# Kernel tuning notes

Hardware: AMD Instinct MI355X
Metric: run time of the kernel (lower is better)

## Reference

```python
import jax, jax.numpy as jnp
import numpy as np

GAMMA = 0.96875
SCALE_BASE = 512.0


def _fixed_pos_embedding(scale):
    # scale: (L, d) where d = head_dim // 2
    L, d = scale.shape
    inv_freq = 1.0 / (10000.0 ** (jnp.arange(d, dtype=jnp.float32) / d))
    sinusoid = jnp.arange(L, dtype=jnp.float32)[:, None] * inv_freq  # (L, d)
    return jnp.sin(sinusoid), jnp.cos(sinusoid)


def _rotate_every_two(x):
    # (..., D) -> (..., D) with pairs (x0, x1) -> (-x1, x0)
    x1 = x[..., ::2]
    x2 = x[..., 1::2]
    return jnp.stack((-x2, x1), axis=-1).reshape(x.shape)


def _dup_interleave(m):
    # (L, d) -> (L, 2d), each column duplicated (matches rotary pairing)
    return jnp.repeat(m, 2, axis=-1)


def xpos(x, offset=0, downscale=False):
    # x: (B, S, D). Standard torchscale-style XPos rotary embedding.
    S, D = x.shape[-2], x.shape[-1]
    scale_vec = (jnp.arange(0, D, 2, dtype=jnp.float32) + 0.4 * D) / (1.4 * D)  # (D/2,)
    min_pos = -(S + offset) // 2
    max_pos = S + offset + min_pos
    power = jnp.arange(min_pos, max_pos, dtype=jnp.float32) / SCALE_BASE  # (S+offset,)
    scale = scale_vec ** power[:, None]  # (S+offset, D/2)
    sin, cos = _fixed_pos_embedding(scale)
    if scale.shape[0] > S:  # keep the last S positions
        scale, sin, cos = scale[-S:], sin[-S:], cos[-S:]
    if downscale:
        scale = 1.0 / scale
    sin = _dup_interleave(sin * scale)  # (S, D)
    cos = _dup_interleave(cos * scale)  # (S, D)
    return x * cos + _rotate_every_two(x) * sin


def _decay_mask(S, dtype):
    # D[n, m] = gamma^(n-m) if n >= m else 0  (lower triangular)
    m = jnp.arange(S)
    diff = m[:, None] - m  # (S, S)
    causal = diff >= 0
    exp = jnp.where(causal, diff, 0).astype(dtype)
    return jnp.where(causal, jnp.asarray(GAMMA, dtype) ** exp, jnp.zeros((), dtype))


def setup_inputs() -> dict:
    key = jax.random.key(0)
    kx, kq, kk, kv = jax.random.split(key, 4)
    B, S, H, Dh = 4, 4096, 2048, 256
    return {
        "x": jax.random.normal(kx, (B, S, H), dtype=jnp.float32),
        "w_q": jax.random.normal(kq, (H, Dh), dtype=jnp.float32),
        "w_k": jax.random.normal(kk, (H, Dh), dtype=jnp.float32),
        "w_v": jax.random.normal(kv, (H, Dh), dtype=jnp.float32),
    }


def reference(x, w_q, w_k, w_v):
    # x: (B, S, H) -> out: (B, S, Dh)
    B, S, _ = x.shape
    decay = _decay_mask(S, x.dtype)[None]  # (1, S, S)
    q = xpos(x @ w_q)                       # (B, S, Dh)
    k = xpos(x @ w_k, downscale=True)       # (B, S, Dh)
    v = x @ w_v                             # (B, S, Dh)
    ret = jnp.einsum("bsd,btd->bst", q, k) * decay  # (B, S, S)
    return jnp.einsum("bst,btd->bsd", ret, v)       # (B, S, Dh)
```

## Files before the change

kernel.cpp:

```cpp
#include <hip/hip_runtime.h>
#include <cstddef>
#include <cstdint>

#define Bn 4
#define Sn 4096
#define Hn 2048
#define Dn 256

typedef float f32x16 __attribute__((ext_vector_type(16)));
typedef short bf16x8 __attribute__((ext_vector_type(8)));

#define AS3 __attribute__((address_space(3)))
#define AS1 __attribute__((address_space(1)))

#define L2G -0.045803689613125f
#define GC 2.9526131e-4f

__device__ __forceinline__ unsigned short f2bf(float f) {
  union { float f; unsigned int u; } a; a.f = f;
  unsigned int r = a.u + 0x7fffu + ((a.u >> 16) & 1u);
  return (unsigned short)(r >> 16);
}
__device__ __forceinline__ float bf2f(unsigned int b) {
  union { unsigned int u; float f; } a; a.u = b << 16;
  return a.f;
}

__global__ __launch_bounds__(256) void prep_kernel(const float* __restrict__ wq,
                                                   const float* __restrict__ wk,
                                                   const float* __restrict__ wv,
                                                   unsigned short* __restrict__ wt,
                                                   float* __restrict__ rt) {
  __shared__ __align__(16) unsigned short T[64][72];
  const int bx = blockIdx.x;
  const int tid = threadIdx.x;
  if (bx < 2048) {
    const int g = bx * 256 + tid;
    const int s = g >> 7;
    const int jp = g & 127;
    const float invf = exp2f((float)jp * (-13.287712379549449f / 128.0f));
    float sn, cs;
    sincosf((float)s * invf, &sn, &cs);
    const float l2sv = log2f((2.0f * jp + 102.4f) * (1.0f / 358.4f));
    const float pw = ((float)s - 2048.0f) * (1.0f / 512.0f);
    const float tl = (float)(s & 255) * L2G;
    const float ex = pw * l2sv + tl;
    const float eq = exp2f(ex), ek = exp2f(-ex);
    float2* q = (float2*)rt;
    float2* k = (float2*)(rt + 4096 * 256);
    q[(size_t)s * 128 + jp] = make_float2(cs * eq, sn * eq);
    k[(size_t)s * 128 + jp] = make_float2(cs * ek, sn * ek);
  } else {
    const int bw = bx - 2048;
    const int k0 = (bw & 31) * 64;
    const int n0 = (bw >> 5) * 64;
    const float* w = (n0 < 256) ? wq : (n0 < 512 ? wk : wv);
    const int nc0 = n0 & 255;
#pragma unroll
    for (int it = 0; it < 2; ++it) {
      int flat = it * 256 + tid;
      int r = flat >> 3, c8 = flat & 7;
      const float* src = w + (size_t)(k0 + r) * 256 + nc0 + c8 * 8;
      float4 v0 = *(const float4*)src;
      float4 v1 = *(const float4*)(src + 4);
      T[c8 * 8 + 0][r] = f2bf(v0.x); T[c8 * 8 + 1][r] = f2bf(v0.y);
      T[c8 * 8 + 2][r] = f2bf(v0.z); T[c8 * 8 + 3][r] = f2bf(v0.w);
      T[c8 * 8 + 4][r] = f2bf(v1.x); T[c8 * 8 + 5][r] = f2bf(v1.y);
      T[c8 * 8 + 6][r] = f2bf(v1.z); T[c8 * 8 + 7][r] = f2bf(v1.w);
    }
    __syncthreads();
#pragma unroll
    for (int it = 0; it < 2; ++it) {
      int flat = it * 256 + tid;
      int nr = flat >> 3, kc8 = flat & 7;
      int n = n0 + nr;
      int kc_sw = kc8 ^ (n & 7);
      uint4 val = *(const uint4*)&T[nr][kc8 * 8];
      *(uint4*)((char*)wt + (size_t)n * 4096 + (size_t)k0 * 2 + kc_sw * 16) = val;
    }
  }
}

__global__ __launch_bounds__(512, 2) void proj6_kernel(const float* __restrict__ x,
                                                       const unsigned short* __restrict__ wt,
                                                       const float* __restrict__ rt,
                                                       unsigned short* __restrict__ qkv,
                                                       unsigned short* __restrict__ kt,
                                                       unsigned short* __restrict__ vt) {
  __shared__ __align__(16) char smem[49152];
  unsigned short* As = (unsigned short*)smem;
  const int tid = threadIdx.x;
  const int lane = tid & 63;
  const int wid = tid >> 6;
  const int wr = wid >> 2, wc = wid & 3;
  const int m0 = blockIdx.x * 128;
  const int kind = blockIdx.y;
  const int l31 = lane & 31, lh = lane >> 5;

  const int arow = tid >> 2;
  const int acg = (tid & 3) << 4;
  const int asw = (arow & 7) << 4;

  f32x16 acc[2][2];
#pragma unroll
  for (int i = 0; i < 2; ++i)
#pragma unroll
    for (int j = 0; j < 2; ++j) acc[i][j] = 0.0f;

  for (int k0 = 0; k0 < Hn; k0 += 64) {
    const float* srcA = x + (size_t)(m0 + arow) * 2048 + k0 + acg;
    float4 f0 = ((const float4*)srcA)[0];
    float4 f1 = ((const float4*)srcA)[1];
    float4 f2 = ((const float4*)srcA)[2];
    float4 f3 = ((const float4*)srcA)[3];
    {
      AS3 char* ldsb = (AS3 char*)(smem + 16384);
#pragma unroll
      for (int i = 0; i < 4; ++i) {
        int ou = i * 8192 + wid * 1024;
        int o = ou + lane * 16;
        int row = o >> 7, colB = o & 127;
        const char* srcB = (const char*)wt + (size_t)(kind * 256 + row) * 4096 + k0 * 2 + colB;
        __builtin_amdgcn_global_load_lds((const AS1 unsigned int*)srcB,
                                         (AS3 unsigned int*)(ldsb + ou), 16, 0, 0);
      }
    }
    {
      uint4 u0, u1;
      asm("v_cvt_pk_bf16_f32 %0, %1, %2" : "=v"(u0.x) : "v"(f0.x), "v"(f0.y));
      asm("v_cvt_pk_bf16_f32 %0, %1, %2" : "=v"(u0.y) : "v"(f0.z), "v"(f0.w));
      asm("v_cvt_pk_bf16_f32 %0, %1, %2" : "=v"(u0.z) : "v"(f1.x), "v"(f1.y));
      asm("v_cvt_pk_bf16_f32 %0, %1, %2" : "=v"(u0.w) : "v"(f1.z), "v"(f1.w));
      asm("v_cvt_pk_bf16_f32 %0, %1, %2" : "=v"(u1.x) : "v"(f2.x), "v"(f2.y));
      asm("v_cvt_pk_bf16_f32 %0, %1, %2" : "=v"(u1.y) : "v"(f2.z), "v"(f2.w));
      asm("v_cvt_pk_bf16_f32 %0, %1, %2" : "=v"(u1.z) : "v"(f3.x), "v"(f3.y));
      asm("v_cvt_pk_bf16_f32 %0, %1, %2" : "=v"(u1.w) : "v"(f3.z), "v"(f3.w));
      *(uint4*)((char*)As + arow * 128 + ((acg * 2) ^ asw)) = u0;
      *(uint4*)((char*)As + arow * 128 + ((acg * 2 + 16) ^ asw)) = u1;
    }
    __syncthreads();
#pragma unroll
    for (int kc = 0; kc < 4; ++kc) {
      const int kb = kc * 32 + lh * 16;
      bf16x8 a[2], b[2];
#pragma unroll
      for (int i = 0; i < 2; ++i) {
        int mr = wr * 64 + i * 32 + l31;
        a[i] = *(const bf16x8*)((const char*)As + mr * 128 + (kb ^ ((mr & 7) << 4)));
        int nr = wc * 64 + i * 32 + l31;
        b[i] = *(const bf16x8*)(smem + 16384 + nr * 128 + (kb ^ ((nr & 7) << 4)));
      }
#pragma unroll
      for (int i = 0; i < 2; ++i)
#pragma unroll
        for (int j = 0; j < 2; ++j)
          acc[i][j] = __builtin_amdgcn_mfma_f32_32x32x16_bf16(a[i], b[j], acc[i][j], 0, 0, 0);
    }
    __syncthreads();
  }

  const int bidx = m0 >> 12;
  const int t0b = m0 & 4095;

  if (kind < 2) {
    const float* rtb = rt + (size_t)kind * (4096 * 256);
    int jp[2];
#pragma unroll
    for (int j = 0; j < 2; ++j) jp[j] = (wc * 64 + j * 32 + l31) >> 1;
    const int odd = l31 & 1;
#pragma unroll
    for (int i = 0; i < 2; ++i)
#pragma unroll
      for (int reg = 0; reg < 16; ++reg) {
        const int mm = m0 + wr * 64 + i * 32 + (reg & 3) + 8 * (reg >> 2) + 4 * lh;
        const int s = mm & (Sn - 1);
#pragma unroll
        for (int j = 0; j < 2; ++j) {
          const float2 cf = *(const float2*)(rtb + (size_t)s * 256 + jp[j] * 2);
          float v = acc[i][j][reg];
          float p = __shfl_xor(v, 1, 64);
          acc[i][j][reg] = odd ? (v * cf.x + p * cf.y) : (v * cf.x - p * cf.y);
        }
      }
  }

  if (kind == 0) {
#pragma unroll
    for (int i = 0; i < 2; ++i)
#pragma unroll
      for (int j = 0; j < 2; ++j)
#pragma unroll
        for (int reg = 0; reg < 16; ++reg) {
          int m = m0 + wr * 64 + i * 32 + (reg & 3) + 8 * (reg >> 2) + 4 * lh;
          int n = wc * 64 + j * 32 + l31;
          qkv[(size_t)m * 768 + n] = f2bf(acc[i][j][reg]);
        }
  } else {
    if (kind == 1) {
#pragma unroll
      for (int i = 0; i < 2; ++i)
#pragma unroll
        for (int j = 0; j < 2; ++j)
#pragma unroll
          for (int reg = 0; reg < 16; ++reg) {
            int m = m0 + wr * 64 + i * 32 + (reg & 3) + 8 * (reg >> 2) + 4 * lh;
            int d = wc * 64 + j * 32 + l31;
            qkv[(size_t)m * 768 + 256 + (d ^ ((m & 7) << 3))] = f2bf(acc[i][j][reg]);
          }
    }
    unsigned short* dst = (kind == 1) ? kt : vt;
#pragma unroll
    for (int h = 0; h < 2; ++h) {
      __syncthreads();
      if ((wc >> 1) == h) {
#pragma unroll
        for (int i = 0; i < 2; ++i)
#pragma unroll
          for (int j = 0; j < 2; ++j) {
            const int dl = (wc & 1) * 64 + j * 32 + l31;
#pragma unroll
            for (int k8 = 0; k8 < 8; ++k8) {
              const int r0 = 2 * k8;
              const int t = wr * 64 + i * 32 + (r0 & 3) + 8 * (r0 >> 2) + 4 * lh;
              unsigned int pk;
              asm("v_cvt_pk_bf16_f32 %0, %1, %2" : "=v"(pk)
                  : "v"(acc[i][j][r0]), "v"(acc[i][j][r0 + 1]));
              *(unsigned int*)(smem + dl * 256 + ((2 * t) ^ ((dl & 7) << 4))) = pk;
            }
          }
      }
      __syncthreads();
#pragma unroll
      for (int p = 0; p < 4; ++p) {
        const int fl = p * 512 + tid;
        const int dl = fl >> 4, t8 = fl & 15;
        uint4 val = *(const uint4*)(smem + dl * 256 + ((t8 * 16) ^ ((dl & 7) << 4)));
        *(uint4*)(dst + (size_t)(bidx * 256 + h * 128 + dl) * 4096 + t0b + t8 * 8) = val;
      }
    }
  }
}

__global__ __launch_bounds__(256) void wt_build(const float* __restrict__ wq,
                                                const float* __restrict__ wk,
                                                const float* __restrict__ wv,
                                                unsigned short* __restrict__ wt) {
  __shared__ __align__(16) unsigned short T[64][72];
  const int tid = threadIdx.x;
  const int k0 = blockIdx.x * 64;
  const int n0 = blockIdx.y * 64;
  const float* w = (n0 < 256) ? wq : (n0 < 512 ? wk : wv);
  const int nc0 = n0 & 255;
#pragma unroll
  for (int it = 0; it < 2; ++it) {
    int flat = it * 256 + tid;
    int r = flat >> 3, c8 = flat & 7;
    const float* src = w + (size_t)(k0 + r) * 256 + nc0 + c8 * 8;
    float4 v0 = *(const float4*)src;
    float4 v1 = *(const float4*)(src + 4);
    T[c8 * 8 + 0][r] = f2bf(v0.x); T[c8 * 8 + 1][r] = f2bf(v0.y);
    T[c8 * 8 + 2][r] = f2bf(v0.z); T[c8 * 8 + 3][r] = f2bf(v0.w);
    T[c8 * 8 + 4][r] = f2bf(v1.x); T[c8 * 8 + 5][r] = f2bf(v1.y);
    T[c8 * 8 + 6][r] = f2bf(v1.z); T[c8 * 8 + 7][r] = f2bf(v1.w);
  }
  __syncthreads();
#pragma unroll
  for (int it = 0; it < 2; ++it) {
    int flat = it * 256 + tid;
    int nr = flat >> 3, kc8 = flat & 7;
    int n = n0 + nr;
    int kc_sw = kc8 ^ (n & 7);
    uint4 val = *(const uint4*)&T[nr][kc8 * 8];
    *(uint4*)((char*)wt + (size_t)n * 4096 + (size_t)k0 * 2 + kc_sw * 16) = val;
  }
}

__global__ __launch_bounds__(256, 2) void proj_kernel(const float* __restrict__ x,
                                                      const unsigned short* __restrict__ wt,
                                                      unsigned short* __restrict__ qkv) {
  __shared__ __align__(16) unsigned short As[128 * 64];
  __shared__ __align__(16) unsigned short Bs[128 * 64];
  const int tid = threadIdx.x;
  const int lane = tid & 63;
  const int wid = tid >> 6;
  const int wr = wid >> 1, wc = wid & 1;
  const int m0 = blockIdx.x * 128;
  const int n0 = blockIdx.y * 128;
  const int l31 = lane & 31, lh = lane >> 5;

  f32x16 acc[2][2];
#pragma unroll
  for (int i = 0; i < 2; ++i)
#pragma unroll
    for (int j = 0; j < 2; ++j) acc[i][j] = 0.0f;

  for (int k0 = 0; k0 < Hn; k0 += 64) {
    {
      AS3 char* ldsb = (AS3 char*)Bs;
#pragma unroll
      for (int i = 0; i < 4; ++i) {
        int ou = i * 4096 + wid * 1024;
        int o = ou + lane * 16;
        int row = o >> 7, col = o & 127;
        const char* src = (const char*)wt + (size_t)(n0 + row) * 4096 + k0 * 2 + col;
        __builtin_amdgcn_global_load_lds((const AS1 unsigned int*)src,
                                         (AS3 unsigned int*)(ldsb + ou), 16, 0, 0);
      }
    }
#pragma unroll
    for (int i = 0; i < 4; ++i) {
      int o = i * 256 + tid;
      int row = o >> 3, c8 = o & 7;
      const float* src = x + (size_t)(m0 + row) * 2048 + k0 + c8 * 8;
      float4 v0 = *(const float4*)src;
      float4 v1 = *(const float4*)(src + 4);
      uint4 val;
      val.x = f2bf(v0.x) | ((unsigned int)f2bf(v0.y) << 16);
      val.y = f2bf(v0.z) | ((unsigned int)f2bf(v0.w) << 16);
      val.z = f2bf(v1.x) | ((unsigned int)f2bf(v1.y) << 16);
      val.w = f2bf(v1.z) | ((unsigned int)f2bf(v1.w) << 16);
      *(uint4*)((char*)As + row * 128 + ((c8 * 16) ^ ((row & 7) << 4))) = val;
    }
    __syncthreads();
#pragma unroll
    for (int kc = 0; kc < 4; ++kc) {
      const int kb = kc * 32 + lh * 16;
      bf16x8 a[2], b[2];
#pragma unroll
      for (int i = 0; i < 2; ++i) {
        int mr = wr * 64 + i * 32 + l31;
        a[i] = *(const bf16x8*)((const char*)As + mr * 128 + (kb ^ ((mr & 7) << 4)));
        int nr = wc * 64 + i * 32 + l31;
        b[i] = *(const bf16x8*)((const char*)Bs + nr * 128 + (kb ^ ((nr & 7) << 4)));
      }
#pragma unroll
      for (int i = 0; i < 2; ++i)
#pragma unroll
        for (int j = 0; j < 2; ++j)
          acc[i][j] = __builtin_amdgcn_mfma_f32_32x32x16_bf16(a[i], b[j], acc[i][j], 0, 0, 0);
    }
    __syncthreads();
  }
  const bool khalf = (n0 >= 256 && n0 < 512);
#pragma unroll
  for (int i = 0; i < 2; ++i)
#pragma unroll
    for (int j = 0; j < 2; ++j)
#pragma unroll
      for (int reg = 0; reg < 16; ++reg) {
        int m = m0 + wr * 64 + i * 32 + (reg & 3) + 8 * (reg >> 2) + 4 * lh;
        int n = n0 + wc * 64 + j * 32 + l31;
        if (khalf) n = 256 + ((n - 256) ^ ((m & 7) << 3));
        qkv[(size_t)m * 768 + n] = f2bf(acc[i][j][reg]);
      }
}

__global__ __launch_bounds__(256) void xpos_kernel(unsigned short* __restrict__ qkv) {
  const int g = blockIdx.x * 256 + threadIdx.x;
  const int m = g >> 5;
  const int c = g & 31;
  const float s = (float)(m & (Sn - 1));
  unsigned short* qrow = qkv + (size_t)m * 768;
  const int csw = c ^ (m & 7);
  uint4 qv = *(uint4*)(qrow + c * 8);
  uint4 kv = *(uint4*)(qrow + 256 + csw * 8);
  unsigned int* qu = (unsigned int*)&qv;
  unsigned int* ku = (unsigned int*)&kv;
  const float pw = (s - 2048.0f) * (1.0f / 512.0f);
  const float gp = exp2f((float)(m & 255) * L2G);
#pragma unroll
  for (int p = 0; p < 4; ++p) {
    const int jp = c * 4 + p;
    const float invf = exp2f((float)jp * (-13.287712379549449f / 128.0f));
    float sn, cs;
    sincosf(s * invf, &sn, &cs);
    const float sv = (2.0f * jp + 102.4f) * (1.0f / 358.4f);
    const float scq = exp2f(pw * log2f(sv)) * gp;
    const float sci = 1.0f / scq;
    float q0 = bf2f(qu[p] & 0xffffu), q1 = bf2f(qu[p] >> 16);
    float k0 = bf2f(ku[p] & 0xffffu), k1 = bf2f(ku[p] >> 16);
    float q0r = (q0 * cs - q1 * sn) * scq;
    float q1r = (q1 * cs + q0 * sn) * scq;
    float k0r = (k0 * cs - k1 * sn) * sci;
    float k1r = (k1 * cs + k0 * sn) * sci;
    qu[p] = f2bf(q0r) | ((unsigned int)f2bf(q1r) << 16);
    ku[p] = f2bf(k0r) | ((unsigned int)f2bf(k1r) << 16);
  }
  *(uint4*)(qrow + c * 8) = qv;
  *(uint4*)(qrow + 256 + csw * 8) = kv;
}

__global__ __launch_bounds__(256) void kvt_build(const unsigned short* __restrict__ qkv,
                                                 unsigned short* __restrict__ kt,
                                                 unsigned short* __restrict__ vt) {
  __shared__ __align__(16) unsigned short Tk[64][72];
  __shared__ __align__(16) unsigned short Tv[64][72];
  const int tid = threadIdx.x;
  const int t0 = blockIdx.x * 64;
  const int d0 = blockIdx.y * 64;
  const int b = blockIdx.z;
  const size_t rowb = ((size_t)b * Sn + t0) * 1536;
#pragma unroll
  for (int it = 0; it < 2; ++it) {
    int flat = it * 256 + tid;
    int r = flat >> 3, c8 = flat & 7;
    int kc = (d0 >> 3) + c8;
    int kcs = kc ^ (r & 7);
    uint4 kvv = *(const uint4*)((const char*)qkv + rowb + (size_t)r * 1536 + 512 + kcs * 16);
    uint4 vvv = *(const uint4*)((const char*)qkv + rowb + (size_t)r * 1536 + 1024 + (size_t)(d0 + c8 * 8) * 2);
    const unsigned short* ke = (const unsigned short*)&kvv;
    const unsigned short* ve = (const unsigned short*)&vvv;
#pragma unroll
    for (int e = 0; e < 8; ++e) { Tk[c8 * 8 + e][r] = ke[e]; Tv[c8 * 8 + e][r] = ve[e]; }
  }
  __syncthreads();
#pragma unroll
  for (int it = 0; it < 2; ++it) {
    int flat = it * 256 + tid;
    int dr = flat >> 3, tc8 = flat & 7;
    *(uint4*)(kt + (size_t)(b * 256 + d0 + dr) * 4096 + t0 + tc8 * 8) = *(const uint4*)&Tk[dr][tc8 * 8];
    *(uint4*)(vt + (size_t)(b * 256 + d0 + dr) * 4096 + t0 + tc8 * 8) = *(const uint4*)&Tv[dr][tc8 * 8];
  }
}

__global__ __launch_bounds__(256) void mbuild_kernel(const unsigned short* __restrict__ kt,
                                                     const unsigned short* __restrict__ vt,
                                                     unsigned short* __restrict__ mt) {
  const int tid = threadIdx.x;
  const int lane = tid & 63;
  const int wid = tid >> 6;
  const int l31 = lane & 31, lh = lane >> 5;
  const int jc = blockIdx.x;
  const int quad = blockIdx.y;
  const int b = blockIdx.z;
  const int d2w = ((quad >> 1) * 2 + (wid >> 1)) * 64;
  const int d1w = ((quad & 1) * 2 + (wid & 1)) * 64;
  const size_t tb = (size_t)jc * 256;

  f32x16 acc[2][2];
#pragma unroll
  for (int i = 0; i < 2; ++i)
#pragma unroll
    for (int j = 0; j < 2; ++j) acc[i][j] = 0.0f;

#pragma unroll 2
  for (int dc = 0; dc < 16; ++dc) {
    const int ko = dc * 32 + lh * 16;
    bf16x8 a[2], bb[2];
#pragma unroll
    for (int i = 0; i < 2; ++i) {
      a[i]  = *(const bf16x8*)((const char*)vt + ((size_t)(b * 256 + d2w + i * 32 + l31) * 4096 + tb) * 2 + ko);
      bb[i] = *(const bf16x8*)((const char*)kt + ((size_t)(b * 256 + d1w + i * 32 + l31) * 4096 + tb) * 2 + ko);
    }
#pragma unroll
    for (int i = 0; i < 2; ++i)
#pragma unroll
      for (int j = 0; j < 2; ++j)
        acc[i][j] = __builtin_amdgcn_mfma_f32_32x32x16_bf16(a[i], bb[j], acc[i][j], 0, 0, 0);
  }
  unsigned short* dst = mt + ((size_t)(b * 16 + jc) << 16);
#pragma unroll
  for (int i = 0; i < 2; ++i)
#pragma unroll
    for (int j = 0; j < 2; ++j)
#pragma unroll
      for (int reg = 0; reg < 16; ++reg) {
        int row = d2w + i * 32 + (reg & 3) + 8 * (reg >> 2) + 4 * lh;
        int col = d1w + j * 32 + l31;
        dst[row * 256 + col] = f2bf(acc[i][j][reg]);
      }
}

__global__ __launch_bounds__(256) void scan_kernel(unsigned short* __restrict__ mt) {
  const int e0 = (blockIdx.x * 256 + threadIdx.x) * 4;
  const int b = blockIdx.y;
  unsigned short* base = mt + ((size_t)b << 20);
  float s0 = 0.f, s1 = 0.f, s2 = 0.f, s3 = 0.f;
  for (int j = 1; j < 16; ++j) {
    unsigned short* p = base + ((size_t)(j - 1) << 16) + e0;
    uint2 mv = *(const uint2*)p;
    s0 = GC * (s0 + bf2f(mv.x & 0xffffu));
    s1 = GC * (s1 + bf2f(mv.x >> 16));
    s2 = GC * (s2 + bf2f(mv.y & 0xffffu));
    s3 = GC * (s3 + bf2f(mv.y >> 16));
    uint2 w;
    w.x = f2bf(s0) | ((unsigned int)f2bf(s1) << 16);
    w.y = f2bf(s2) | ((unsigned int)f2bf(s3) << 16);
    *(uint2*)p = w;
  }
}

__global__ __launch_bounds__(256, 2) void retc_kernel(const unsigned short* __restrict__ qkv,
                                                      const unsigned short* __restrict__ vt,
                                                      const unsigned short* __restrict__ mt,
                                                      float* __restrict__ out) {
  __shared__ float cmb[2][32][128];
  const int tid = threadIdx.x;
  const int lane = tid & 63;
  const int tw = tid >> 6;
  const int l31 = lane & 31, lh = lane >> 5;
  const int st = blockIdx.x;
  const int dh = blockIdx.y;
  const int b = blockIdx.z;
  const int j = st >> 3;
  const int base = st & ~7;
  const int s0 = st * 32;
  const int d0 = dh * 128;

  bf16x8 qf[16];
  {
    const char* qrow = (const char*)qkv + ((size_t)b * Sn + s0 + l31) * 1536;
#pragma unroll
    for (int dc = 0; dc < 16; ++dc)
      qf[dc] = *(const bf16x8*)(qrow + dc * 32 + lh * 16);
  }

  f32x16 acc[4];
#pragma unroll
  for (int i = 0; i < 4; ++i) acc[i] = 0.0f;

  if (j > 0) {
    const char* Sj = (const char*)mt + ((size_t)(b * 16 + j - 1) << 17);
#pragma unroll
    for (int dcl = 0; dcl < 4; ++dcl) {
      const int dc = tw * 4 + dcl;
#pragma unroll
      for (int g = 0; g < 4; ++g) {
        const int d2 = d0 + g * 32 + l31;
        bf16x8 sbf = *(const bf16x8*)(Sj + (size_t)d2 * 512 + dc * 32 + lh * 16);
        acc[g] = __builtin_amdgcn_mfma_f32_32x32x16_bf16(qf[dc], sbf, acc[g], 0, 0, 0);
      }
    }
  }

  const int sg = s0 + l31;
  const int ksw = (l31 & 7) << 4;
  for (int tt = base; tt <= st; ++tt) {
    if (((tt - base) & 3) != tw) continue;
    const bool msk = (tt == st);
    const int t0 = tt * 32;

    f32x16 sacc = 0.0f;
    const char* krow = (const char*)qkv + ((size_t)b * Sn + t0 + l31) * 1536 + 512;
    __builtin_amdgcn_s_setprio(1);
#pragma unroll
    for (int dc = 0; dc < 16; ++dc) {
      bf16x8 kf = *(const bf16x8*)(krow + ((dc * 32 + lh * 16) ^ ksw));
      sacc = __builtin_amdgcn_mfma_f32_32x32x16_bf16(kf, qf[dc], sacc, 0, 0, 0);
    }
    __builtin_amdgcn_s_setprio(0);

    unsigned int P[8];
#pragma unroll
    for (int k = 0; k < 8; ++k) {
      const int r0 = 2 * k;
      float f0 = sacc[r0], f1 = sacc[r0 + 1];
      if (msk) {
        const int tg0 = t0 + (r0 & 3) + 8 * (r0 >> 2) + 4 * lh;
        f0 = (sg - tg0 >= 0) ? f0 : 0.0f;
        f1 = (sg - tg0 - 1 >= 0) ? f1 : 0.0f;
      }
      unsigned int pk;
      asm("v_cvt_pk_bf16_f32 %0, %1, %2" : "=v"(pk) : "v"(f0), "v"(f1));
      P[k] = pk;
    }
    asm volatile("v_permlane32_swap_b32 %0, %1" : "+v"(P[0]), "+v"(P[2]));
    asm volatile("v_permlane32_swap_b32 %0, %1" : "+v"(P[1]), "+v"(P[3]));
    asm volatile("v_permlane32_swap_b32 %0, %1" : "+v"(P[4]), "+v"(P[6]));
    asm volatile("v_permlane32_swap_b32 %0, %1" : "+v"(P[5]), "+v"(P[7]));

    __builtin_amdgcn_s_setprio(1);
#pragma unroll
    for (int kc = 0; kc < 2; ++kc) {
      uint4 pw;
      pw.x = P[kc * 4 + 0]; pw.y = P[kc * 4 + 1];
      pw.z = P[kc * 4 + 2]; pw.w = P[kc * 4 + 3];
      bf16x8 pf = *(const bf16x8*)&pw;
#pragma unroll
      for (int g = 0; g < 4; ++g) {
        const int d = d0 + g * 32 + l31;
        bf16x8 vf = *(const bf16x8*)((const char*)vt +
            ((size_t)(b * 256 + d) * 4096 + t0) * 2 + kc * 32 + lh * 16);
        acc[g] = __builtin_amdgcn_mfma_f32_32x32x16_bf16(pf, vf, acc[g], 0, 0, 0);
      }
    }
    __builtin_amdgcn_s_setprio(0);
  }

  if (tw >= 2) {
#pragma unroll
    for (int g = 0; g < 4; ++g)
#pragma unroll
      for (int reg = 0; reg < 16; ++reg) {
        int sl = (reg & 3) + 8 * (reg >> 2) + 4 * lh;
        cmb[tw - 2][sl][g * 32 + l31] = acc[g][reg];
      }
  }
  __syncthreads();
  if (tw < 2) {
#pragma unroll
    for (int g = 0; g < 4; ++g)
#pragma unroll
      for (int reg = 0; reg < 16; ++reg) {
        int sl = (reg & 3) + 8 * (reg >> 2) + 4 * lh;
        acc[g][reg] += cmb[tw][sl][g * 32 + l31];
      }
  }
  __syncthreads();
  if (tw == 1) {
#pragma unroll
    for (int g = 0; g < 4; ++g)
#pragma unroll
      for (int reg = 0; reg < 16; ++reg) {
        int sl = (reg & 3) + 8 * (reg >> 2) + 4 * lh;
        cmb[0][sl][g * 32 + l31] = acc[g][reg];
      }
  }
  __syncthreads();
  if (tw == 0) {
#pragma unroll
    for (int g = 0; g < 4; ++g)
#pragma unroll
      for (int reg = 0; reg < 16; ++reg) {
        int sl = (reg & 3) + 8 * (reg >> 2) + 4 * lh;
        int c = g * 32 + l31;
        out[((size_t)(b * Sn + s0 + sl)) * 256 + d0 + c] = acc[g][reg] + cmb[0][sl][c];
      }
  }
}

extern "C" void kernel_launch(void* const* d_in, const int* in_sizes, int n_in,
                              void* d_out, int out_size, void* d_ws, size_t ws_size,
                              hipStream_t stream) {
  (void)in_sizes; (void)n_in; (void)out_size;
  const float* x  = (const float*)d_in[0];
  const float* wq = (const float*)d_in[1];
  const float* wk = (const float*)d_in[2];
  const float* wv = (const float*)d_in[3];
  float* out = (float*)d_out;
  char* ws = (char*)d_ws;

  unsigned short* qkv = (unsigned short*)(ws);
  unsigned short* vt  = (unsigned short*)(ws + 25165824);
  unsigned short* kt  = (unsigned short*)(ws + 33554432);
  unsigned short* mt  = (unsigned short*)(ws + 41943040);

  const size_t NEED_BIG = 128974848;
  if (ws_size >= NEED_BIG) {
    unsigned short* wt = (unsigned short*)(ws + 117440512);
    float*          rtab = (float*)(ws + 120586240);
    prep_kernel<<<2432, 256, 0, stream>>>(wq, wk, wv, wt, rtab);
    proj6_kernel<<<dim3(128, 3), 512, 0, stream>>>(x, wt, rtab, qkv, kt, vt);
  } else {
    unsigned short* wt = (unsigned short*)(ws + 41943040);
    wt_build<<<dim3(32, 12), 256, 0, stream>>>(wq, wk, wv, wt);
    proj_kernel<<<dim3(128, 6), 256, 0, stream>>>(x, wt, qkv);
    xpos_kernel<<<2048, 256, 0, stream>>>(qkv);
    kvt_build<<<dim3(64, 4, 4), 256, 0, stream>>>(qkv, kt, vt);
  }
  mbuild_kernel<<<dim3(16, 4, 4), 256, 0, stream>>>(kt, vt, mt);
  scan_kernel<<<dim3(64, 4), 256, 0, stream>>>(mt);
  retc_kernel<<<dim3(128, 2, 4), 256, 0, stream>>>(qkv, vt, mt, out);
}
```

Measured before the change: 162.2 us.

## Prefetch next x tile into registers and use finer waitcnt in projection loop

The projection GEMM loop now loads the next iteration's fp32 x row slice into registers while the current one is converted and consumed. The two full __syncthreads are replaced with manual s_waitcnt vmcnt(4) plus raw barriers, and the MFMA section is wrapped in s_setprio. The aim is to hide global load latency of the A operand behind compute without adding LDS double-buffering. The cost is more VGPRs under a 512x2 launch bound, and correctness depends on the hand-written wait counts matching the order in which loads are issued.

Result: slower. 212.8 us (+31.2%).

```diff
diff --git a/kernel.cpp b/kernel.cpp
--- a/kernel.cpp
+++ b/kernel.cpp
@@ -81,7 +81,7 @@
   }
 }
 
-__global__ __launch_bounds__(512, 2) void proj6_kernel(const float* __restrict__ x,
+__global__ __launch_bounds__(512, 2) void proj7_kernel(const float* __restrict__ x,
                                                        const unsigned short* __restrict__ wt,
                                                        const float* __restrict__ rt,
                                                        unsigned short* __restrict__ qkv,
@@ -100,6 +100,7 @@
   const int arow = tid >> 2;
   const int acg = (tid & 3) << 4;
   const int asw = (arow & 7) << 4;
+  const float* arowp = x + (size_t)(m0 + arow) * 2048 + acg;
 
   f32x16 acc[2][2];
 #pragma unroll
@@ -107,12 +108,14 @@
 #pragma unroll
     for (int j = 0; j < 2; ++j) acc[i][j] = 0.0f;
 
-  for (int k0 = 0; k0 < Hn; k0 += 64) {
-    const float* srcA = x + (size_t)(m0 + arow) * 2048 + k0 + acg;
-    float4 f0 = ((const float4*)srcA)[0];
-    float4 f1 = ((const float4*)srcA)[1];
-    float4 f2 = ((const float4*)srcA)[2];
-    float4 f3 = ((const float4*)srcA)[3];
+  float4 c0, c1, c2, c3;
+  {
+    const float4* s = (const float4*)arowp;
+    c0 = s[0]; c1 = s[1]; c2 = s[2]; c3 = s[3];
+  }
+
+  for (int t = 0; t < 32; ++t) {
+    const int k0 = t << 6;
     {
       AS3 char* ldsb = (AS3 char*)(smem + 16384);
 #pragma unroll
@@ -125,20 +128,31 @@
                                          (AS3 unsigned int*)(ldsb + ou), 16, 0, 0);
       }
     }
+    __builtin_amdgcn_sched_barrier(0);
+    const int kn = ((t + 1) & 31) << 6;
+    float4 n0v, n1v, n2v, n3v;
+    {
+      const float4* s = (const float4*)(arowp + kn);
+      n0v = s[0]; n1v = s[1]; n2v = s[2]; n3v = s[3];
+    }
+    __builtin_amdgcn_sched_barrier(0);
     {
       uint4 u0, u1;
-      asm("v_cvt_pk_bf16_f32 %0, %1, %2" : "=v"(u0.x) : "v"(f0.x), "v"(f0.y));
-      asm("v_cvt_pk_bf16_f32 %0, %1, %2" : "=v"(u0.y) : "v"(f0.z), "v"(f0.w));
-      asm("v_cvt_pk_bf16_f32 %0, %1, %2" : "=v"(u0.z) : "v"(f1.x), "v"(f1.y));
-      asm("v_cvt_pk_bf16_f32 %0, %1, %2" : "=v"(u0.w) : "v"(f1.z), "v"(f1.w));
-      asm("v_cvt_pk_bf16_f32 %0, %1, %2" : "=v"(u1.x) : "v"(f2.x), "v"(f2.y));
-      asm("v_cvt_pk_bf16_f32 %0, %1, %2" : "=v"(u1.y) : "v"(f2.z), "v"(f2.w));
-      asm("v_cvt_pk_bf16_f32 %0, %1, %2" : "=v"(u1.z) : "v"(f3.x), "v"(f3.y));
-      asm("v_cvt_pk_bf16_f32 %0, %1, %2" : "=v"(u1.w) : "v"(f3.z), "v"(f3.w));
+      asm("v_cvt_pk_bf16_f32 %0, %1, %2" : "=v"(u0.x) : "v"(c0.x), "v"(c0.y));
+      asm("v_cvt_pk_bf16_f32 %0, %1, %2" : "=v"(u0.y) : "v"(c0.z), "v"(c0.w));
+      asm("v_cvt_pk_bf16_f32 %0, %1, %2" : "=v"(u0.z) : "v"(c1.x), "v"(c1.y));
+      asm("v_cvt_pk_bf16_f32 %0, %1, %2" : "=v"(u0.w) : "v"(c1.z), "v"(c1.w));
+      asm("v_cvt_pk_bf16_f32 %0, %1, %2" : "=v"(u1.x) : "v"(c2.x), "v"(c2.y));
+      asm("v_cvt_pk_bf16_f32 %0, %1, %2" : "=v"(u1.y) : "v"(c2.z), "v"(c2.w));
+      asm("v_cvt_pk_bf16_f32 %0, %1, %2" : "=v"(u1.z) : "v"(c3.x), "v"(c3.y));
+      asm("v_cvt_pk_bf16_f32 %0, %1, %2" : "=v"(u1.w) : "v"(c3.z), "v"(c3.w));
       *(uint4*)((char*)As + arow * 128 + ((acg * 2) ^ asw)) = u0;
       *(uint4*)((char*)As + arow * 128 + ((acg * 2 + 16) ^ asw)) = u1;
     }
-    __syncthreads();
+    asm volatile("s_waitcnt vmcnt(4) lgkmcnt(0)" ::: "memory");
+    __builtin_amdgcn_s_barrier();
+    __builtin_amdgcn_sched_barrier(0);
+    __builtin_amdgcn_s_setprio(1);
 #pragma unroll
     for (int kc = 0; kc < 4; ++kc) {
       const int kb = kc * 32 + lh * 16;
@@ -156,8 +170,13 @@
         for (int j = 0; j < 2; ++j)
           acc[i][j] = __builtin_amdgcn_mfma_f32_32x32x16_bf16(a[i], b[j], acc[i][j], 0, 0, 0);
     }
-    __syncthreads();
-  }
+    __builtin_amdgcn_s_setprio(0);
+    __builtin_amdgcn_s_barrier();
+    __builtin_amdgcn_sched_barrier(0);
+    c0 = n0v; c1 = n1v; c2 = n2v; c3 = n3v;
+  }
+  asm volatile("s_waitcnt vmcnt(0)" ::: "memory");
+  __syncthreads();
 
   const int bidx = m0 >> 12;
   const int t0b = m0 & 4095;
@@ -221,11 +240,11 @@
 #pragma unroll
             for (int k8 = 0; k8 < 8; ++k8) {
               const int r0 = 2 * k8;
-              const int t = wr * 64 + i * 32 + (r0 & 3) + 8 * (r0 >> 2) + 4 * lh;
+              const int tt = wr * 64 + i * 32 + (r0 & 3) + 8 * (r0 >> 2) + 4 * lh;
               unsigned int pk;
               asm("v_cvt_pk_bf16_f32 %0, %1, %2" : "=v"(pk)
                   : "v"(acc[i][j][r0]), "v"(acc[i][j][r0 + 1]));
-              *(unsigned int*)(smem + dl * 256 + ((2 * t) ^ ((dl & 7) << 4))) = pk;
+              *(unsigned int*)(smem + dl * 256 + ((2 * tt) ^ ((dl & 7) << 4))) = pk;
             }
           }
       }
@@ -650,7 +669,7 @@
     unsigned short* wt = (unsigned short*)(ws + 117440512);
     float*          rtab = (float*)(ws + 120586240);
     prep_kernel<<<2432, 256, 0, stream>>>(wq, wk, wv, wt, rtab);
-    proj6_kernel<<<dim3(128, 3), 512, 0, stream>>>(x, wt, rtab, qkv, kt, vt);
+    proj7_kernel<<<dim3(128, 3), 512, 0, stream>>>(x, wt, rtab, qkv, kt, vt);
   } else {
     unsigned short* wt = (unsigned short*)(ws + 41943040);
     wt_build<<<dim3(32, 12), 256, 0, stream>>>(wq, wk, wv, wt);
```
